# Optimization experiments

Hardware: AMD Instinct MI355X
Metric: run time of the kernel (lower is better)

Reference implementation:

```python
import jax, jax.numpy as jnp
import numpy as np

DIM = 768
NUM_HEADS = 12
HEAD_DIM = DIM // NUM_HEADS
SCALE = HEAD_DIM ** -0.5


def setup_inputs() -> dict:
    key = jax.random.key(0)
    k1, k2, k3, k4 = jax.random.split(key, 4)
    B, N, C = 4, 2048, DIM
    x = jax.random.normal(k1, (B, N, C), dtype=jnp.float32)
    # nn.Linear(dim, 3*dim, bias=False): weight shape (3C, C), y = x @ W^T
    w_qkv = jax.random.normal(k2, (3 * C, C), dtype=jnp.float32) * (C ** -0.5)
    # nn.Linear(dim, dim) with default bias=True
    w_proj = jax.random.normal(k3, (C, C), dtype=jnp.float32) * (C ** -0.5)
    b_proj = jax.random.normal(k4, (C,), dtype=jnp.float32) * 0.02
    return {"x": x, "w_qkv": w_qkv, "w_proj": w_proj, "b_proj": b_proj}


def reference(x, w_qkv, w_proj, b_proj):
    B, N, C = x.shape
    H, D = NUM_HEADS, HEAD_DIM
    qkv = jnp.einsum('bnc,oc->bno', x, w_qkv)  # (B, N, 3C)
    qkv = qkv.reshape(B, N, 3, H, D).transpose(2, 0, 3, 1, 4)  # (3, B, H, N, D)
    q, k, v = qkv[0], qkv[1], qkv[2]
    attn = jnp.einsum('bhnd,bhmd->bhnm', q, k) * jnp.float32(SCALE)  # (B,H,N,N)
    attn = jax.nn.softmax(attn, axis=-1)
    out = jnp.einsum('bhnm,bhmd->bhnd', attn, v)  # (B,H,N,D)
    out = out.transpose(0, 2, 1, 3).reshape(B, N, C)
    out = jnp.einsum('bnc,oc->bno', out, w_proj) + b_proj
    return out
```

## Files before the change

kernel.cpp:

```cpp
#include <hip/hip_runtime.h>
#include <math.h>

#define B_ 4
#define N_ 2048
#define C_ 768
#define H_ 12
#define D_ 64
#define QKSCALE_ 0.18033688011112042f

typedef unsigned short u16;
typedef unsigned int u32;
typedef short s16x8 __attribute__((ext_vector_type(8)));
typedef float f32x4 __attribute__((ext_vector_type(4)));
typedef u32 u32x2 __attribute__((ext_vector_type(2)));

__device__ __forceinline__ u16 f2bf(float f) {
    union { float f; u32 u; } v; v.f = f;
    u32 r = (v.u + 0x7fffu + ((v.u >> 16) & 1u)) >> 16;
    return (u16)r;
}

__device__ __forceinline__ u32 pkbf(float a, float b) {
    union { float f; u32 u; } ua, ub; ua.f = a; ub.f = b;
    u32 ra = ua.u + 0x7fffu + ((ua.u >> 16) & 1u);
    u32 rb = ub.u + 0x7fffu + ((ub.u >> 16) & 1u);
    return __builtin_amdgcn_perm(rb, ra, 0x07060302u);
}

__device__ __forceinline__ void gl_lds16(const u16* g, u16* l) {
    __builtin_amdgcn_global_load_lds(
        (__attribute__((address_space(1))) void*)g,
        (__attribute__((address_space(3))) void*)l, 16, 0, 0);
}

#define NX4_  (B_ * N_ * C_ / 4)
#define NWQ4_ (3 * C_ * C_ / 4)
#define NWP4_ (C_ * C_ / 4)
__global__ __launch_bounds__(256) void cvt_all(const float4* __restrict__ x,
                                               const float4* __restrict__ wq,
                                               const float4* __restrict__ wp,
                                               ushort4* __restrict__ xb,
                                               ushort4* __restrict__ wqb,
                                               ushort4* __restrict__ wpb)
{
    const int tot = NX4_ + NWQ4_ + NWP4_;
    int i = blockIdx.x * blockDim.x + threadIdx.x;
    const int stride = gridDim.x * blockDim.x;
    for (; i < tot; i += stride) {
        const float4* s; ushort4* d; int j;
        if (i < NX4_)              { s = x;  d = xb;  j = i; }
        else if (i < NX4_ + NWQ4_) { s = wq; d = wqb; j = i - NX4_; }
        else                       { s = wp; d = wpb; j = i - NX4_ - NWQ4_; }
        float4 v = s[j];
        ushort4 o;
        o.x = f2bf(v.x); o.y = f2bf(v.y); o.z = f2bf(v.z); o.w = f2bf(v.w);
        d[j] = o;
    }
}

template<int BM, int WPEU, bool OUT_BF16, bool BIAS, bool QSCALE>
__global__ __launch_bounds__(256, WPEU) void gemm_mfma(const u16* __restrict__ A,
                                                       const u16* __restrict__ Bm,
                                                       const float* __restrict__ bias,
                                                       void* __restrict__ Cout,
                                                       int M, int N, int K)
{
    constexpr int MF  = BM / 32;
    constexpr int AC  = BM / 32;
    constexpr int ASZ = BM * 64, BSZ = 128 * 64;
    __shared__ __align__(16) u16 As[2 * ASZ];
    __shared__ __align__(16) u16 Bs[2 * BSZ];
    const int tid  = threadIdx.x;
    const int wv   = tid >> 6;
    const int lane = tid & 63;
    const int lr   = lane & 15;
    const int lq   = lane >> 4;
    const int wm   = (wv >> 1) * (BM / 2);
    const int wn   = (wv & 1) * 64;
    const int row0 = blockIdx.y * BM, col0 = blockIdx.x * 128;

    f32x4 acc[MF][4];
    #pragma unroll
    for (int i = 0; i < MF; i++)
        #pragma unroll
        for (int j = 0; j < 4; j++) { f32x4 z = {0.f,0.f,0.f,0.f}; acc[i][j] = z; }

    const int srow   = lane >> 3;
    const int schunk = ((lane & 7) ^ srow) * 8;

    const int arow_base = (BM / 4) * wv;
    const u16* gA = A + (size_t)(row0 + arow_base + srow) * K + schunk;
    const u16* gB = Bm + (size_t)(col0 + 32 * wv + srow) * K + schunk;
    const int aoff = arow_base * 64;
    const int boff = (32 * wv) * 64;

    const int nIter = K / 64;

    #pragma unroll
    for (int c = 0; c < AC; c++)
        gl_lds16(gA + (size_t)(8 * c) * K, As + aoff + c * 8 * 64);
    #pragma unroll
    for (int c = 0; c < 4; c++)
        gl_lds16(gB + (size_t)(8 * c) * K, Bs + boff + c * 8 * 64);

    for (int t = 0; t < nIter; t++) {
        const int cur = t & 1;
        __syncthreads();
        if (t + 1 < nIter) {
            const int k1 = (t + 1) * 64;
            const int nb = cur ^ 1;
            #pragma unroll
            for (int c = 0; c < AC; c++)
                gl_lds16(gA + (size_t)(8 * c) * K + k1, As + nb * ASZ + aoff + c * 8 * 64);
            #pragma unroll
            for (int c = 0; c < 4; c++)
                gl_lds16(gB + (size_t)(8 * c) * K + k1, Bs + nb * BSZ + boff + c * 8 * 64);
        }
        const u16* __restrict__ Ac = As + cur * ASZ;
        const u16* __restrict__ Bc = Bs + cur * BSZ;
        #pragma unroll
        for (int kk = 0; kk < 2; kk++) {
            const int fo = ((4 * kk + lq) ^ (lr & 7)) * 8;
            s16x8 af[MF], bfr[4];
            #pragma unroll
            for (int i = 0; i < MF; i++)
                af[i] = *(const s16x8*)&Ac[(wm + 16*i + lr) * 64 + fo];
            #pragma unroll
            for (int j = 0; j < 4; j++)
                bfr[j] = *(const s16x8*)&Bc[(wn + 16*j + lr) * 64 + fo];
            #pragma unroll
            for (int i = 0; i < MF; i++)
                #pragma unroll
                for (int j = 0; j < 4; j++)
                    acc[i][j] = __builtin_amdgcn_mfma_f32_16x16x32_bf16(af[i], bfr[j], acc[i][j], 0, 0, 0);
        }
    }

    #pragma unroll
    for (int i = 0; i < MF; i++) {
        #pragma unroll
        for (int j = 0; j < 4; j++) {
            const int col = col0 + wn + 16*j + lr;
            float bv = BIAS ? bias[col] : 0.f;
            #pragma unroll
            for (int r = 0; r < 4; r++) {
                const int row = row0 + wm + 16*i + lq*4 + r;
                float v = acc[i][j][r] + bv;
                if (QSCALE && col < C_) v *= QKSCALE_;
                if (OUT_BF16) ((u16*)Cout)[(size_t)row * N + col] = f2bf(v);
                else          ((float*)Cout)[(size_t)row * N + col] = v;
            }
        }
    }
}

__global__ __launch_bounds__(256, 3) void attn_mfma(const u16* __restrict__ qkv,
                                                    u16* __restrict__ attout)
{
    __shared__ __align__(16) u16 Ks[2][64 * 64];
    __shared__ __align__(16) u16 Vt[2][64][72];
    __shared__ __align__(16) u16 Ps[128 * 64];

    const int tid  = threadIdx.x;
    const int wv   = tid >> 6;
    const int lane = tid & 63;
    const int lr   = lane & 15;
    const int lq   = lane >> 4;
    const int n0   = blockIdx.x * 128;
    const int bh   = blockIdx.y, b = bh / H_, h = bh % H_;
    const size_t rs = 3 * C_;

    const u16* Qg = qkv + ((size_t)b * N_ + n0) * rs + h * D_;
    const u16* Kg = qkv + ((size_t)b * N_) * rs + C_ + h * D_;
    const u16* Vg = Kg + C_;

    s16x8 qf[2][2];
    #pragma unroll
    for (int iq = 0; iq < 2; iq++)
        #pragma unroll
        for (int kk = 0; kk < 2; kk++)
            qf[iq][kk] = *(const s16x8*)(Qg + (size_t)(32*wv + 16*iq + lr) * rs + kk*32 + lq*8);

    f32x4 oacc[2][4];
    float li[2] = {0.f, 0.f};
    #pragma unroll
    for (int i = 0; i < 2; i++)
        #pragma unroll
        for (int j = 0; j < 4; j++) { f32x4 z = {0.f,0.f,0.f,0.f}; oacc[i][j] = z; }

    const int skey = tid >> 2;
    const int sc0  = (tid & 3) * 2;
    const int scA  = (sc0     ^ (skey & 7)) * 8;
    const int scB  = ((sc0+1) ^ (skey & 7)) * 8;
    const int vc = tid & 7, vp = tid >> 3;
    const int vkey0 = 2 * vp, vd0 = vc * 8;
    const int vcol0 = (vkey0 + 8 * vc) & 63;

    s16x8 kr0, kr1, vr0, vr1;
    {
        const u16* kp = Kg + (size_t)skey * rs + sc0 * 8;
        kr0 = *(const s16x8*)kp; kr1 = *(const s16x8*)(kp + 8);
        const u16* vp2 = Vg + (size_t)vkey0 * rs + vd0;
        vr0 = *(const s16x8*)vp2; vr1 = *(const s16x8*)(vp2 + rs);
    }
    *(s16x8*)&Ks[0][skey * 64 + scA] = kr0;
    *(s16x8*)&Ks[0][skey * 64 + scB] = kr1;
    #pragma unroll
    for (int u = 0; u < 8; u++) {
        u32 pk = (u32)(u16)vr0[u] | ((u32)(u16)vr1[u] << 16);
        *(u32*)&Vt[0][vd0 + u][vcol0] = pk;
    }
    {
        const u16* kp = Kg + (size_t)(64 + skey) * rs + sc0 * 8;
        kr0 = *(const s16x8*)kp; kr1 = *(const s16x8*)(kp + 8);
        const u16* vp2 = Vg + (size_t)(64 + vkey0) * rs + vd0;
        vr0 = *(const s16x8*)vp2; vr1 = *(const s16x8*)(vp2 + rs);
    }

    const int NT = N_ / 64;
    for (int t = 0; t < NT; t++) {
        const int cur = t & 1, nxt = cur ^ 1;
        __syncthreads();
        if (t + 1 < NT) {
            *(s16x8*)&Ks[nxt][skey * 64 + scA] = kr0;
            *(s16x8*)&Ks[nxt][skey * 64 + scB] = kr1;
            #pragma unroll
            for (int u = 0; u < 8; u++) {
                u32 pk = (u32)(u16)vr0[u] | ((u32)(u16)vr1[u] << 16);
                *(u32*)&Vt[nxt][vd0 + u][vcol0] = pk;
            }
        }
        if (t + 2 < NT) {
            const u16* kp = Kg + (size_t)((t+2)*64 + skey) * rs + sc0 * 8;
            kr0 = *(const s16x8*)kp; kr1 = *(const s16x8*)(kp + 8);
            const u16* vp2 = Vg + (size_t)((t+2)*64 + vkey0) * rs + vd0;
            vr0 = *(const s16x8*)vp2; vr1 = *(const s16x8*)(vp2 + rs);
        }

        f32x4 st[4][2];
        #pragma unroll
        for (int jk = 0; jk < 4; jk++)
            #pragma unroll
            for (int iq = 0; iq < 2; iq++) { f32x4 z = {0.f,0.f,0.f,0.f}; st[jk][iq] = z; }
        #pragma unroll
        for (int kk = 0; kk < 2; kk++) {
            s16x8 kf[4];
            #pragma unroll
            for (int jk = 0; jk < 4; jk++)
                kf[jk] = *(const s16x8*)&Ks[cur][(16*jk + lr) * 64 + ((4*kk + lq) ^ (lr & 7)) * 8];
            #pragma unroll
            for (int jk = 0; jk < 4; jk++) {
                st[jk][0] = __builtin_amdgcn_mfma_f32_16x16x32_bf16(kf[jk], qf[0][kk], st[jk][0], 0, 0, 0);
                st[jk][1] = __builtin_amdgcn_mfma_f32_16x16x32_bf16(kf[jk], qf[1][kk], st[jk][1], 0, 0, 0);
            }
        }

        #pragma unroll
        for (int jk = 0; jk < 4; jk++)
            #pragma unroll
            for (int iq = 0; iq < 2; iq++) {
                const float p0 = __builtin_amdgcn_exp2f(st[jk][iq][0]);
                const float p1 = __builtin_amdgcn_exp2f(st[jk][iq][1]);
                const float p2 = __builtin_amdgcn_exp2f(st[jk][iq][2]);
                const float p3 = __builtin_amdgcn_exp2f(st[jk][iq][3]);
                li[iq] += (p0 + p1) + (p2 + p3);
                u32x2 w;
                w.x = pkbf(p0, p1);
                w.y = pkbf(p2, p3);
                const int prow = 32*wv + 16*iq + lr;
                const int pch  = ((2*jk + (lq >> 1)) ^ (lr & 7)) * 8 + (lq & 1) * 4;
                *(u32x2*)&Ps[prow * 64 + pch] = w;
            }

        #pragma unroll
        for (int kk = 0; kk < 2; kk++) {
            s16x8 ap0 = *(const s16x8*)&Ps[(32*wv      + lr) * 64 + ((4*kk + lq) ^ (lr & 7)) * 8];
            s16x8 ap1 = *(const s16x8*)&Ps[(32*wv + 16 + lr) * 64 + ((4*kk + lq) ^ (lr & 7)) * 8];
            #pragma unroll
            for (int j2 = 0; j2 < 4; j2++) {
                const int pb = ((kk*4 + lq) + 2*j2 + (lr >> 3)) & 7;
                s16x8 bv = *(const s16x8*)&Vt[cur][16*j2 + lr][pb * 8];
                oacc[0][j2] = __builtin_amdgcn_mfma_f32_16x16x32_bf16(ap0, bv, oacc[0][j2], 0, 0, 0);
                oacc[1][j2] = __builtin_amdgcn_mfma_f32_16x16x32_bf16(ap1, bv, oacc[1][j2], 0, 0, 0);
            }
        }
    }

    #pragma unroll
    for (int iq = 0; iq < 2; iq++) {
        li[iq] += __shfl_xor(li[iq], 16);
        li[iq] += __shfl_xor(li[iq], 32);
    }
    #pragma unroll
    for (int iq = 0; iq < 2; iq++) {
        #pragma unroll
        for (int r = 0; r < 4; r++) {
            const float inv = 1.f / __shfl(li[iq], 4*lq + r);
            const int row = n0 + 32*wv + 16*iq + 4*lq + r;
            #pragma unroll
            for (int j2 = 0; j2 < 4; j2++)
                attout[((size_t)(b * N_ + row)) * C_ + h * D_ + 16*j2 + lr] =
                    f2bf(oacc[iq][j2][r] * inv);
        }
    }
}

extern "C" void kernel_launch(void* const* d_in, const int* in_sizes, int n_in,
                              void* d_out, int out_size, void* d_ws, size_t ws_size,
                              hipStream_t stream) {
    const float* x      = (const float*)d_in[0];
    const float* w_qkv  = (const float*)d_in[1];
    const float* w_proj = (const float*)d_in[2];
    const float* b_proj = (const float*)d_in[3];
    float* out = (float*)d_out;

    const int NX   = B_ * N_ * C_;
    const int NWQ  = 3 * C_ * C_;
    const int NWP  = C_ * C_;
    const int NQKV = B_ * N_ * 3 * C_;

    u16* xb   = (u16*)d_ws;
    u16* wqb  = xb + NX;
    u16* wpb  = wqb + NWQ;
    u16* qkvb = wpb + NWP;
    u16* attb = qkvb + NQKV;

    dim3 blk(256);

    cvt_all<<<768, blk, 0, stream>>>((const float4*)x, (const float4*)w_qkv,
                                     (const float4*)w_proj,
                                     (ushort4*)xb, (ushort4*)wqb, (ushort4*)wpb);

    const int M = B_ * N_;
    gemm_mfma<128, 2, true, false, true><<<dim3((3*C_)/128, M/128), blk, 0, stream>>>(
        xb, wqb, nullptr, qkvb, M, 3*C_, C_);

    attn_mfma<<<dim3(N_/128, B_ * H_), blk, 0, stream>>>(qkvb, attb);

    gemm_mfma<64, 3, false, true, false><<<dim3(C_/128, M/64), blk, 0, stream>>>(
        attb, wpb, b_proj, out, M, C_, C_);
}
```

Baseline: 217.8 us.

## Switch attention to 32x32x16 MFMA and keep P in registers via permlane swap

The attention kernel moves from 16x16x32 to 32x32x16 bf16 MFMA tiles for both QK^T and PV. The probability tile is no longer staged through shared memory. It is converted with v_cvt_pk_bf16_f32 and rearranged across lane halves with v_permlane32_swap, so it can feed the PV MFMA directly. This removes the Ps LDS buffer and its writes and reads and frees LDS for occupancy. The cost is larger accumulator register footprint, inline asm that is specific to gfx950, and a changed final normalization layout.

```diff
diff --git a/kernel.cpp b/kernel.cpp
--- a/kernel.cpp
+++ b/kernel.cpp
@@ -12,19 +12,12 @@
 typedef unsigned int u32;
 typedef short s16x8 __attribute__((ext_vector_type(8)));
 typedef float f32x4 __attribute__((ext_vector_type(4)));
-typedef u32 u32x2 __attribute__((ext_vector_type(2)));
+typedef float f32x16 __attribute__((ext_vector_type(16)));
 
 __device__ __forceinline__ u16 f2bf(float f) {
     union { float f; u32 u; } v; v.f = f;
     u32 r = (v.u + 0x7fffu + ((v.u >> 16) & 1u)) >> 16;
     return (u16)r;
-}
-
-__device__ __forceinline__ u32 pkbf(float a, float b) {
-    union { float f; u32 u; } ua, ub; ua.f = a; ub.f = b;
-    u32 ra = ua.u + 0x7fffu + ((ua.u >> 16) & 1u);
-    u32 rb = ub.u + 0x7fffu + ((ub.u >> 16) & 1u);
-    return __builtin_amdgcn_perm(rb, ra, 0x07060302u);
 }
 
 __device__ __forceinline__ void gl_lds16(const u16* g, u16* l) {
@@ -159,13 +152,12 @@
 {
     __shared__ __align__(16) u16 Ks[2][64 * 64];
     __shared__ __align__(16) u16 Vt[2][64][72];
-    __shared__ __align__(16) u16 Ps[128 * 64];
 
     const int tid  = threadIdx.x;
     const int wv   = tid >> 6;
     const int lane = tid & 63;
-    const int lr   = lane & 15;
-    const int lq   = lane >> 4;
+    const int l31  = lane & 31;
+    const int hi   = lane >> 5;
     const int n0   = blockIdx.x * 128;
     const int bh   = blockIdx.y, b = bh / H_, h = bh % H_;
     const size_t rs = 3 * C_;
@@ -174,19 +166,15 @@
     const u16* Kg = qkv + ((size_t)b * N_) * rs + C_ + h * D_;
     const u16* Vg = Kg + C_;
 
-    s16x8 qf[2][2];
-    #pragma unroll
-    for (int iq = 0; iq < 2; iq++)
-        #pragma unroll
-        for (int kk = 0; kk < 2; kk++)
-            qf[iq][kk] = *(const s16x8*)(Qg + (size_t)(32*wv + 16*iq + lr) * rs + kk*32 + lq*8);
-
-    f32x4 oacc[2][4];
-    float li[2] = {0.f, 0.f};
-    #pragma unroll
-    for (int i = 0; i < 2; i++)
-        #pragma unroll
-        for (int j = 0; j < 4; j++) { f32x4 z = {0.f,0.f,0.f,0.f}; oacc[i][j] = z; }
+    s16x8 qf[4];
+    #pragma unroll
+    for (int kk = 0; kk < 4; kk++)
+        qf[kk] = *(const s16x8*)(Qg + (size_t)(32*wv + l31) * rs + kk*16 + hi*8);
+
+    const f32x16 z16 = {0.f,0.f,0.f,0.f,0.f,0.f,0.f,0.f,
+                        0.f,0.f,0.f,0.f,0.f,0.f,0.f,0.f};
+    f32x16 oacc[2] = {z16, z16};
+    float li = 0.f;
 
     const int skey = tid >> 2;
     const int sc0  = (tid & 3) * 2;
@@ -237,71 +225,64 @@
             vr0 = *(const s16x8*)vp2; vr1 = *(const s16x8*)(vp2 + rs);
         }
 
-        f32x4 st[4][2];
-        #pragma unroll
-        for (int jk = 0; jk < 4; jk++)
-            #pragma unroll
-            for (int iq = 0; iq < 2; iq++) { f32x4 z = {0.f,0.f,0.f,0.f}; st[jk][iq] = z; }
-        #pragma unroll
-        for (int kk = 0; kk < 2; kk++) {
-            s16x8 kf[4];
-            #pragma unroll
-            for (int jk = 0; jk < 4; jk++)
-                kf[jk] = *(const s16x8*)&Ks[cur][(16*jk + lr) * 64 + ((4*kk + lq) ^ (lr & 7)) * 8];
-            #pragma unroll
-            for (int jk = 0; jk < 4; jk++) {
-                st[jk][0] = __builtin_amdgcn_mfma_f32_16x16x32_bf16(kf[jk], qf[0][kk], st[jk][0], 0, 0, 0);
-                st[jk][1] = __builtin_amdgcn_mfma_f32_16x16x32_bf16(kf[jk], qf[1][kk], st[jk][1], 0, 0, 0);
+        #define KF(j, kk) (*(const s16x8*)&Ks[cur][(32*(j) + l31) * 64 + \
+                           ((2*(kk) + hi) ^ (l31 & 7)) * 8])
+        f32x16 st0 = __builtin_amdgcn_mfma_f32_32x32x16_bf16(KF(0,0), qf[0], z16, 0, 0, 0);
+        f32x16 st1 = __builtin_amdgcn_mfma_f32_32x32x16_bf16(KF(1,0), qf[0], z16, 0, 0, 0);
+        #pragma unroll
+        for (int kk = 1; kk < 4; kk++) {
+            st0 = __builtin_amdgcn_mfma_f32_32x32x16_bf16(KF(0,kk), qf[kk], st0, 0, 0, 0);
+            st1 = __builtin_amdgcn_mfma_f32_32x32x16_bf16(KF(1,kk), qf[kk], st1, 0, 0, 0);
+        }
+        #undef KF
+
+        #pragma unroll
+        for (int j = 0; j < 2; j++) {
+            const f32x16 s = j ? st1 : st0;
+            float p[16];
+            #pragma unroll
+            for (int r = 0; r < 16; r++) p[r] = __builtin_amdgcn_exp2f(s[r]);
+            #pragma unroll
+            for (int r = 0; r < 16; r += 4)
+                li += (p[r] + p[r+1]) + (p[r+2] + p[r+3]);
+            u32 w[4][2];
+            #pragma unroll
+            for (int m = 0; m < 4; m++) {
+                asm("v_cvt_pk_bf16_f32 %0, %1, %2"
+                    : "=v"(w[m][0]) : "v"(p[4*m+0]), "v"(p[4*m+1]));
+                asm("v_cvt_pk_bf16_f32 %0, %1, %2"
+                    : "=v"(w[m][1]) : "v"(p[4*m+2]), "v"(p[4*m+3]));
             }
-        }
-
-        #pragma unroll
-        for (int jk = 0; jk < 4; jk++)
-            #pragma unroll
-            for (int iq = 0; iq < 2; iq++) {
-                const float p0 = __builtin_amdgcn_exp2f(st[jk][iq][0]);
-                const float p1 = __builtin_amdgcn_exp2f(st[jk][iq][1]);
-                const float p2 = __builtin_amdgcn_exp2f(st[jk][iq][2]);
-                const float p3 = __builtin_amdgcn_exp2f(st[jk][iq][3]);
-                li[iq] += (p0 + p1) + (p2 + p3);
-                u32x2 w;
-                w.x = pkbf(p0, p1);
-                w.y = pkbf(p2, p3);
-                const int prow = 32*wv + 16*iq + lr;
-                const int pch  = ((2*jk + (lq >> 1)) ^ (lr & 7)) * 8 + (lq & 1) * 4;
-                *(u32x2*)&Ps[prow * 64 + pch] = w;
+            #pragma unroll
+            for (int h2 = 0; h2 < 2; h2++) {
+                asm("v_permlane32_swap_b32 %0, %1"
+                    : "+v"(w[2*h2][0]), "+v"(w[2*h2+1][0]));
+                asm("v_permlane32_swap_b32 %0, %1"
+                    : "+v"(w[2*h2][1]), "+v"(w[2*h2+1][1]));
+                const int sp = 2*j + h2;
+                union { u32 uw[4]; s16x8 v; } pa;
+                pa.uw[0] = w[2*h2][0];   pa.uw[1] = w[2*h2][1];
+                pa.uw[2] = w[2*h2+1][0]; pa.uw[3] = w[2*h2+1][1];
+                #pragma unroll
+                for (int j2 = 0; j2 < 2; j2++) {
+                    const int pb = (2*sp + hi + 4*j2 + (l31 >> 3)) & 7;
+                    s16x8 vb = *(const s16x8*)&Vt[cur][32*j2 + l31][pb * 8];
+                    oacc[j2] = __builtin_amdgcn_mfma_f32_32x32x16_bf16(pa.v, vb, oacc[j2], 0, 0, 0);
+                }
             }
-
-        #pragma unroll
-        for (int kk = 0; kk < 2; kk++) {
-            s16x8 ap0 = *(const s16x8*)&Ps[(32*wv      + lr) * 64 + ((4*kk + lq) ^ (lr & 7)) * 8];
-            s16x8 ap1 = *(const s16x8*)&Ps[(32*wv + 16 + lr) * 64 + ((4*kk + lq) ^ (lr & 7)) * 8];
-            #pragma unroll
-            for (int j2 = 0; j2 < 4; j2++) {
-                const int pb = ((kk*4 + lq) + 2*j2 + (lr >> 3)) & 7;
-                s16x8 bv = *(const s16x8*)&Vt[cur][16*j2 + lr][pb * 8];
-                oacc[0][j2] = __builtin_amdgcn_mfma_f32_16x16x32_bf16(ap0, bv, oacc[0][j2], 0, 0, 0);
-                oacc[1][j2] = __builtin_amdgcn_mfma_f32_16x16x32_bf16(ap1, bv, oacc[1][j2], 0, 0, 0);
-            }
-        }
-    }
-
-    #pragma unroll
-    for (int iq = 0; iq < 2; iq++) {
-        li[iq] += __shfl_xor(li[iq], 16);
-        li[iq] += __shfl_xor(li[iq], 32);
-    }
-    #pragma unroll
-    for (int iq = 0; iq < 2; iq++) {
-        #pragma unroll
-        for (int r = 0; r < 4; r++) {
-            const float inv = 1.f / __shfl(li[iq], 4*lq + r);
-            const int row = n0 + 32*wv + 16*iq + 4*lq + r;
-            #pragma unroll
-            for (int j2 = 0; j2 < 4; j2++)
-                attout[((size_t)(b * N_ + row)) * C_ + h * D_ + 16*j2 + lr] =
-                    f2bf(oacc[iq][j2][r] * inv);
-        }
+        }
+    }
+
+    li += __shfl_xor(li, 32);
+    const float inv = 1.f / li;
+    #pragma unroll
+    for (int r = 0; r < 16; r++) {
+        const int qr = (r & 3) + 8 * (r >> 2) + 4 * hi;
+        const float iv = __shfl(inv, qr);
+        const size_t grow = (size_t)(b * N_ + n0 + 32*wv + qr);
+        #pragma unroll
+        for (int j2 = 0; j2 < 2; j2++)
+            attout[grow * C_ + h * D_ + 32*j2 + l31] = f2bf(oacc[j2][r] * iv);
     }
 }
 
```

Result: faster. 210.7 us (-3.3%).
